# Kernel optimization log

Measured on AMD Instinct MI355X. Metric: run time of the kernel, lower is better.

The kernel has to match this reference:

```python
import jax, jax.numpy as jnp
import numpy as np

# NF4 codebook used by bitsandbytes (16 levels, normalized to [-1, 1])
NF4_CODE = jnp.array([
    -1.0, -0.6961928009986877, -0.5250730514526367, -0.39491748809814453,
    -0.28444138169288635, -0.18477343022823334, -0.09105003625154495, 0.0,
    0.07958029955625534, 0.16093020141124725, 0.24611230194568634,
    0.33791524171829224, 0.44070982933044434, 0.5626170039176941,
    0.7229568362236023, 1.0], dtype=jnp.float32)
BLOCKSIZE = 64  # bitsandbytes default 4-bit blocksize


def nf4_quant_dequant(w):
    """Simulate bnb NF4 quantize -> dequantize (per-block absmax scaling)."""
    shape = w.shape
    flat = w.reshape(-1, BLOCKSIZE)                     # [n_blocks, 64]
    absmax = jnp.max(jnp.abs(flat), axis=1, keepdims=True)
    normalized = flat / jnp.where(absmax == 0, 1.0, absmax)
    # nearest-codebook-value quantization via midpoint boundaries
    bounds = (NF4_CODE[:-1] + NF4_CODE[1:]) * 0.5       # [15]
    idx = jnp.searchsorted(bounds, normalized)          # [n_blocks, 64] in [0,15]
    return (NF4_CODE[idx] * absmax).reshape(shape)


def setup_inputs() -> dict:
    key = jax.random.key(0)
    k1, k2, k3, kx = jax.random.split(key, 4)
    D, H = 4096, 11008
    scale = 0.02  # typical transformer init scale
    w1 = jax.random.normal(k1, (H, D), jnp.float32) * scale
    w2 = jax.random.normal(k2, (H, D), jnp.float32) * scale
    w3 = jax.random.normal(k3, (D, H), jnp.float32) * scale
    x = jax.random.normal(kx, (2, 2048, D), jnp.float32)
    return {"x": x, "w1": w1, "w2": w2, "w3": w3}


def reference(x, w1, w2, w3):
    dq1 = nf4_quant_dequant(w1)   # [H, D]
    dq2 = nf4_quant_dequant(w2)   # [H, D]
    dq3 = nf4_quant_dequant(w3)   # [D, H]
    gate = jnp.einsum('bsd,hd->bsh', x, dq1)
    up = jnp.einsum('bsd,hd->bsh', x, dq2)
    h = jax.nn.silu(gate) * up
    return jnp.einsum('bsh,dh->bsd', h, dq3)
```

## Files before the change

### kernel.cpp

```cpp
#include <hip/hip_runtime.h>
#include <math.h>

typedef __attribute__((ext_vector_type(4))) float f32x4;
typedef __attribute__((ext_vector_type(8))) short bf16x8;

#define DI __device__ __forceinline__

DI unsigned short f32_to_bf16(float f) {
  unsigned int u = __float_as_uint(f);
  u += 0x7FFFu + ((u >> 16) & 1u);
  return (unsigned short)(u >> 16);
}

static constexpr float kCode[16] = {
    -1.0f, -0.6961928009986877f, -0.5250730514526367f, -0.39491748809814453f,
    -0.28444138169288635f, -0.18477343022823334f, -0.09105003625154495f, 0.0f,
    0.07958029955625534f, 0.16093020141124725f, 0.24611230194568634f,
    0.33791524171829224f, 0.44070982933044434f, 0.5626170039176941f,
    0.7229568362236023f, 1.0f};

__global__ void __launch_bounds__(256) k_dequant_nf4(
    const float* __restrict__ in, unsigned short* __restrict__ out, int n4) {
  int i = blockIdx.x * 256 + threadIdx.x;
  if (i >= n4) return;
  f32x4 v = reinterpret_cast<const f32x4*>(in)[i];
  float am = fmaxf(fmaxf(fabsf(v.x), fabsf(v.y)), fmaxf(fabsf(v.z), fabsf(v.w)));
  am = fmaxf(am, __shfl_xor(am, 1));
  am = fmaxf(am, __shfl_xor(am, 2));
  am = fmaxf(am, __shfl_xor(am, 4));
  am = fmaxf(am, __shfl_xor(am, 8));
  float scale = (am == 0.0f) ? 1.0f : am;
  unsigned short o[4];
#pragma unroll
  for (int j = 0; j < 4; ++j) {
    float nv = ((const float*)&v)[j] / scale;
    int idx = 0;
#pragma unroll
    for (int b = 0; b < 15; ++b)
      idx += (nv > 0.5f * (kCode[b] + kCode[b + 1])) ? 1 : 0;
    o[j] = f32_to_bf16(kCode[idx] * am);
  }
  reinterpret_cast<ushort4*>(out)[i] = make_ushort4(o[0], o[1], o[2], o[3]);
}

__global__ void __launch_bounds__(256) k_f32_to_bf16(
    const float* __restrict__ in, unsigned short* __restrict__ out, int n4) {
  int i = blockIdx.x * 256 + threadIdx.x;
  if (i >= n4) return;
  f32x4 v = reinterpret_cast<const f32x4*>(in)[i];
  reinterpret_cast<ushort4*>(out)[i] =
      make_ushort4(f32_to_bf16(v.x), f32_to_bf16(v.y), f32_to_bf16(v.z), f32_to_bf16(v.w));
}

DI void gload16(const void* g, void* l) {
  __builtin_amdgcn_global_load_lds(
      (const __attribute__((address_space(1))) void*)g,
      (__attribute__((address_space(3))) void*)l, 16, 0, 0);
}

DI void barrier_nodrain() {
  asm volatile("" ::: "memory");
  __builtin_amdgcn_s_barrier();
  asm volatile("" ::: "memory");
}

#define WAITV(N) asm volatile("s_waitcnt vmcnt(" #N ")" ::: "memory")

__global__ void __launch_bounds__(1024, 4) k_gemm_dual_swiglu(
    const unsigned short* __restrict__ X,
    const unsigned short* __restrict__ W1,
    const unsigned short* __restrict__ W2,
    unsigned short* __restrict__ H) {
  constexpr int K = 4096, N = 11008, NK = K / 32;
  __shared__ char ldsb[131072];

  const int tid = threadIdx.x;
  const int w = tid >> 6, l = tid & 63;

  const int bid = blockIdx.x;
  const int lt = (bid & 7) * 172 + (bid >> 3);
  const int mt = lt & 15, nt = lt >> 4;
  const int m0 = mt * 256, n0 = nt * 128;

  const int p = w & 7;
  const bool isGate = (w < 8);
  const int wr = p >> 1, wc = p & 1;

  const int lrow = l >> 2;
  const int kc8 = (((l & 3) ^ ((l >> 3) & 3)) << 3);
  const unsigned short* gsrc0;
  const unsigned short* gsrc1;
  int ldst0;
  if (w < 8) {
    gsrc0 = X + (size_t)(m0 + 32 * w + lrow) * K + kc8;
    gsrc1 = X + (size_t)(m0 + 32 * w + 16 + lrow) * K + kc8;
    ldst0 = 2 * w * 1024;
  } else if (w < 12) {
    gsrc0 = W1 + (size_t)(n0 + 32 * (w - 8) + lrow) * K + kc8;
    gsrc1 = W1 + (size_t)(n0 + 32 * (w - 8) + 16 + lrow) * K + kc8;
    ldst0 = 16384 + (w - 8) * 2048;
  } else {
    gsrc0 = W2 + (size_t)(n0 + 32 * (w - 12) + lrow) * K + kc8;
    gsrc1 = W2 + (size_t)(n0 + 32 * (w - 12) + 16 + lrow) * K + kc8;
    ldst0 = 24576 + (w - 12) * 2048;
  }

#define STG(t) { const int bo_ = (((t) & 3) << 15) + ldst0;          \
    gload16(gsrc0 + (size_t)(t) * 32, ldsb + bo_);                    \
    gload16(gsrc1 + (size_t)(t) * 32, ldsb + bo_ + 1024); }

  const int roff = (((l >> 4) ^ ((l >> 1) & 3)) << 4);
  const char* rdA = ldsb + (wr * 64 + (l & 15)) * 64 + roff;
  const char* rdB = ldsb + 16384 + (isGate ? 0 : 8192) +
                    (wc * 64 + (l & 15)) * 64 + roff;

  f32x4 acc[4][4] = {};

  STG(0); STG(1); STG(2);
  WAITV(4);
  barrier_nodrain();

  for (int t = 0; t < NK; ++t) {
    const int bo = (t & 3) << 15;
    if (t + 3 < NK) STG(t + 3);
    bf16x8 a[4], b[4];
#pragma unroll
    for (int m = 0; m < 4; ++m) a[m] = *(const bf16x8*)(rdA + bo + m * 1024);
#pragma unroll
    for (int n = 0; n < 4; ++n) b[n] = *(const bf16x8*)(rdB + bo + n * 1024);
    __builtin_amdgcn_s_setprio(1);
#pragma unroll
    for (int m = 0; m < 4; ++m)
#pragma unroll
      for (int n = 0; n < 4; ++n)
        acc[m][n] = __builtin_amdgcn_mfma_f32_16x16x32_bf16(a[m], b[n], acc[m][n], 0, 0, 0);
    __builtin_amdgcn_s_setprio(0);
    if (t + 3 < NK)      { WAITV(4); barrier_nodrain(); }
    else if (t + 2 < NK) { WAITV(2); barrier_nodrain(); }
    else if (t + 1 < NK) { WAITV(0); barrier_nodrain(); }
  }
#undef STG

  barrier_nodrain();
  char* xch = ldsb + p * 16384 + (isGate ? 0 : 8192);
#pragma unroll
  for (int m2 = 0; m2 < 2; ++m2)
#pragma unroll
    for (int n = 0; n < 4; ++n) {
      const int m = isGate ? (m2 + 2) : m2;
      *(f32x4*)(xch + ((m2 * 4 + n) * 64 + l) * 16) = acc[m][n];
    }
  barrier_nodrain();
  const char* oxch = ldsb + p * 16384 + (isGate ? 8192 : 0);
  const int er = (l >> 4) * 4, ec = l & 15;
#pragma unroll
  for (int m2 = 0; m2 < 2; ++m2)
#pragma unroll
    for (int n = 0; n < 4; ++n) {
      const int m = isGate ? m2 : (m2 + 2);
      f32x4 other = *(const f32x4*)(oxch + ((m2 * 4 + n) * 64 + l) * 16);
#pragma unroll
      for (int j = 0; j < 4; ++j) {
        const float g_ = isGate ? acc[m][n][j] : other[j];
        const float u_ = isGate ? other[j] : acc[m][n][j];
        const float s = g_ / (1.0f + expf(-g_));
        const int row = m0 + wr * 64 + m * 16 + er + j;
        const int col = n0 + wc * 64 + n * 16 + ec;
        H[(size_t)row * N + col] = f32_to_bf16(s * u_);
      }
    }
}

__global__ void __launch_bounds__(1024, 4) k_gemm_out(
    const unsigned short* __restrict__ Hm,
    const unsigned short* __restrict__ W3,
    float* __restrict__ Out) {
  constexpr int K = 11008, N = 4096, NK = K / 32;
  __shared__ char ldsb[131072];

  const int tid = threadIdx.x;
  const int w = tid >> 6, l = tid & 63;

  const int bid = blockIdx.x;
  const int lt = (bid & 7) * 32 + (bid >> 3);
  const int mt = lt & 15, nt = lt >> 4;
  const int m0 = mt * 256, n0 = nt * 256;

  const int wr = w >> 2, wc = w & 3;

  const int lrow = l >> 2;
  const int kc8 = (((l & 3) ^ ((l >> 3) & 3)) << 3);
  const unsigned short* gsrc0;
  const unsigned short* gsrc1;
  int ldst0;
  if (w < 8) {
    gsrc0 = Hm + (size_t)(m0 + 32 * w + lrow) * K + kc8;
    gsrc1 = Hm + (size_t)(m0 + 32 * w + 16 + lrow) * K + kc8;
    ldst0 = 2 * w * 1024;
  } else {
    gsrc0 = W3 + (size_t)(n0 + 32 * (w - 8) + lrow) * K + kc8;
    gsrc1 = W3 + (size_t)(n0 + 32 * (w - 8) + 16 + lrow) * K + kc8;
    ldst0 = 16384 + (w - 8) * 2048;
  }

#define STG(t) { const int bo_ = (((t) & 3) << 15) + ldst0;          \
    gload16(gsrc0 + (size_t)(t) * 32, ldsb + bo_);                    \
    gload16(gsrc1 + (size_t)(t) * 32, ldsb + bo_ + 1024); }

  const int roff = (((l >> 4) ^ ((l >> 1) & 3)) << 4);
  const char* rdA = ldsb + (wr * 64 + (l & 15)) * 64 + roff;
  const char* rdB = ldsb + 16384 + (wc * 64 + (l & 15)) * 64 + roff;

  f32x4 acc[4][4] = {};

  STG(0); STG(1); STG(2);
  WAITV(4);
  barrier_nodrain();

  for (int t = 0; t < NK; ++t) {
    const int bo = (t & 3) << 15;
    if (t + 3 < NK) STG(t + 3);
    bf16x8 a[4], b[4];
#pragma unroll
    for (int m = 0; m < 4; ++m) a[m] = *(const bf16x8*)(rdA + bo + m * 1024);
#pragma unroll
    for (int n = 0; n < 4; ++n) b[n] = *(const bf16x8*)(rdB + bo + n * 1024);
    __builtin_amdgcn_s_setprio(1);
#pragma unroll
    for (int m = 0; m < 4; ++m)
#pragma unroll
      for (int n = 0; n < 4; ++n)
        acc[m][n] = __builtin_amdgcn_mfma_f32_16x16x32_bf16(a[m], b[n], acc[m][n], 0, 0, 0);
    __builtin_amdgcn_s_setprio(0);
    if (t + 3 < NK)      { WAITV(4); barrier_nodrain(); }
    else if (t + 2 < NK) { WAITV(2); barrier_nodrain(); }
    else if (t + 1 < NK) { WAITV(0); barrier_nodrain(); }
  }
#undef STG

  const int er = (l >> 4) * 4, ec = l & 15;
#pragma unroll
  for (int m = 0; m < 4; ++m)
#pragma unroll
    for (int n = 0; n < 4; ++n) {
      const int row = m0 + wr * 64 + m * 16 + er;
      const int col = n0 + wc * 64 + n * 16 + ec;
      float* ptr = Out + (size_t)row * N + col;
#pragma unroll
      for (int j = 0; j < 4; ++j) ptr[(size_t)j * N] = acc[m][n][j];
    }
}

extern "C" void kernel_launch(void* const* d_in, const int* in_sizes, int n_in,
                              void* d_out, int out_size, void* d_ws, size_t ws_size,
                              hipStream_t stream) {
  const float* x  = (const float*)d_in[0];
  const float* w1 = (const float*)d_in[1];
  const float* w2 = (const float*)d_in[2];
  const float* w3 = (const float*)d_in[3];
  float* out = (float*)d_out;

  char* ws = (char*)d_ws;
  unsigned short* xb  = (unsigned short*)(ws);
  unsigned short* w1b = (unsigned short*)(ws + 33554432);
  unsigned short* w2b = (unsigned short*)(ws + 123731968);
  unsigned short* hb  = (unsigned short*)(ws + 213909504);
  unsigned short* w3b = w1b;

  const int NW = 11008 * 4096 / 4;
  k_f32_to_bf16<<<16384, 256, 0, stream>>>(x, xb, 4096 * 4096 / 4);
  k_dequant_nf4<<<NW / 256, 256, 0, stream>>>(w1, w1b, NW);
  k_dequant_nf4<<<NW / 256, 256, 0, stream>>>(w2, w2b, NW);

  k_gemm_dual_swiglu<<<1376, 1024, 0, stream>>>(xb, w1b, w2b, hb);

  k_dequant_nf4<<<NW / 256, 256, 0, stream>>>(w3, w3b, NW);

  k_gemm_out<<<256, 1024, 0, stream>>>(hb, w3b, out);
}
```

Measured before the change: 1.271 ms.

## Remap GEMM tiles per XCD, peel pipeline epilogue, merge w1/w2 dequant launches

Changes the block-to-tile mapping in both GEMMs so each XCD owns two consecutive M tiles and walks N tiles. The goal is L2 reuse of the activation rows within an XCD, instead of the earlier layout that spread M across XCDs. The main k-loop is peeled so the steady state carries no tail conditionals, and the two weight dequantization kernels are fused into one launch. The new tile order may reduce weight reuse across XCDs, since each XCD now streams all of W1/W2/W3.

New measurement: 1.247 ms. About the same (-1.9%).

```diff
diff --git a/kernel.cpp b/kernel.cpp
--- a/kernel.cpp
+++ b/kernel.cpp
@@ -19,10 +19,7 @@
     0.33791524171829224f, 0.44070982933044434f, 0.5626170039176941f,
     0.7229568362236023f, 1.0f};
 
-__global__ void __launch_bounds__(256) k_dequant_nf4(
-    const float* __restrict__ in, unsigned short* __restrict__ out, int n4) {
-  int i = blockIdx.x * 256 + threadIdx.x;
-  if (i >= n4) return;
+DI void dequant_body(const float* __restrict__ in, unsigned short* __restrict__ out, int i) {
   f32x4 v = reinterpret_cast<const f32x4*>(in)[i];
   float am = fmaxf(fmaxf(fabsf(v.x), fabsf(v.y)), fmaxf(fabsf(v.z), fabsf(v.w)));
   am = fmaxf(am, __shfl_xor(am, 1));
@@ -43,6 +40,24 @@
   reinterpret_cast<ushort4*>(out)[i] = make_ushort4(o[0], o[1], o[2], o[3]);
 }
 
+__global__ void __launch_bounds__(256) k_dequant_nf4(
+    const float* __restrict__ in, unsigned short* __restrict__ out, int n4) {
+  int i = blockIdx.x * 256 + threadIdx.x;
+  if (i >= n4) return;
+  dequant_body(in, out, i);
+}
+
+__global__ void __launch_bounds__(256) k_dequant_nf4_2(
+    const float* __restrict__ in1, const float* __restrict__ in2,
+    unsigned short* __restrict__ out1, unsigned short* __restrict__ out2, int n4) {
+  int i = blockIdx.x * 256 + threadIdx.x;
+  if (i < n4) {
+    dequant_body(in1, out1, i);
+  } else {
+    dequant_body(in2, out2, i - n4);
+  }
+}
+
 __global__ void __launch_bounds__(256) k_f32_to_bf16(
     const float* __restrict__ in, unsigned short* __restrict__ out, int n4) {
   int i = blockIdx.x * 256 + threadIdx.x;
@@ -78,8 +93,9 @@
   const int w = tid >> 6, l = tid & 63;
 
   const int bid = blockIdx.x;
-  const int lt = (bid & 7) * 172 + (bid >> 3);
-  const int mt = lt & 15, nt = lt >> 4;
+  const int xcd = bid & 7, i = bid >> 3;
+  const int nt = i >> 1;
+  const int mt = xcd * 2 + (i & 1);
   const int m0 = mt * 256, n0 = nt * 128;
 
   const int p = w & 7;
@@ -116,29 +132,33 @@
 
   f32x4 acc[4][4] = {};
 
+#define TILE_BODY(bo) {                                                        \
+  bf16x8 a[4], b[4];                                                           \
+  _Pragma("unroll") for (int m = 0; m < 4; ++m)                                \
+    a[m] = *(const bf16x8*)(rdA + (bo) + m * 1024);                            \
+  _Pragma("unroll") for (int n = 0; n < 4; ++n)                                \
+    b[n] = *(const bf16x8*)(rdB + (bo) + n * 1024);                            \
+  __builtin_amdgcn_s_setprio(1);                                               \
+  _Pragma("unroll") for (int m = 0; m < 4; ++m)                                \
+    _Pragma("unroll") for (int n = 0; n < 4; ++n)                              \
+      acc[m][n] = __builtin_amdgcn_mfma_f32_16x16x32_bf16(a[m], b[n], acc[m][n], 0, 0, 0); \
+  __builtin_amdgcn_s_setprio(0); }
+
   STG(0); STG(1); STG(2);
   WAITV(4);
   barrier_nodrain();
 
-  for (int t = 0; t < NK; ++t) {
+  int t = 0;
+  for (; t + 3 < NK; ++t) {
     const int bo = (t & 3) << 15;
-    if (t + 3 < NK) STG(t + 3);
-    bf16x8 a[4], b[4];
-#pragma unroll
-    for (int m = 0; m < 4; ++m) a[m] = *(const bf16x8*)(rdA + bo + m * 1024);
-#pragma unroll
-    for (int n = 0; n < 4; ++n) b[n] = *(const bf16x8*)(rdB + bo + n * 1024);
-    __builtin_amdgcn_s_setprio(1);
-#pragma unroll
-    for (int m = 0; m < 4; ++m)
-#pragma unroll
-      for (int n = 0; n < 4; ++n)
-        acc[m][n] = __builtin_amdgcn_mfma_f32_16x16x32_bf16(a[m], b[n], acc[m][n], 0, 0, 0);
-    __builtin_amdgcn_s_setprio(0);
-    if (t + 3 < NK)      { WAITV(4); barrier_nodrain(); }
-    else if (t + 2 < NK) { WAITV(2); barrier_nodrain(); }
-    else if (t + 1 < NK) { WAITV(0); barrier_nodrain(); }
-  }
+    STG(t + 3);
+    TILE_BODY(bo);
+    WAITV(4); barrier_nodrain();
+  }
+  TILE_BODY((t & 3) << 15); WAITV(2); barrier_nodrain(); ++t;
+  TILE_BODY((t & 3) << 15); WAITV(0); barrier_nodrain(); ++t;
+  TILE_BODY((t & 3) << 15);
+#undef TILE_BODY
 #undef STG
 
   barrier_nodrain();
@@ -157,14 +177,14 @@
   for (int m2 = 0; m2 < 2; ++m2)
 #pragma unroll
     for (int n = 0; n < 4; ++n) {
-      const int m = isGate ? m2 : (m2 + 2);
+      const int mk = isGate ? m2 : (m2 + 2);
       f32x4 other = *(const f32x4*)(oxch + ((m2 * 4 + n) * 64 + l) * 16);
 #pragma unroll
       for (int j = 0; j < 4; ++j) {
-        const float g_ = isGate ? acc[m][n][j] : other[j];
-        const float u_ = isGate ? other[j] : acc[m][n][j];
+        const float g_ = isGate ? acc[mk][n][j] : other[j];
+        const float u_ = isGate ? other[j] : acc[mk][n][j];
         const float s = g_ / (1.0f + expf(-g_));
-        const int row = m0 + wr * 64 + m * 16 + er + j;
+        const int row = m0 + wr * 64 + mk * 16 + er + j;
         const int col = n0 + wc * 64 + n * 16 + ec;
         H[(size_t)row * N + col] = f32_to_bf16(s * u_);
       }
@@ -182,8 +202,9 @@
   const int w = tid >> 6, l = tid & 63;
 
   const int bid = blockIdx.x;
-  const int lt = (bid & 7) * 32 + (bid >> 3);
-  const int mt = lt & 15, nt = lt >> 4;
+  const int xcd = bid & 7, i = bid >> 3;
+  const int nt = i >> 1;
+  const int mt = xcd * 2 + (i & 1);
   const int m0 = mt * 256, n0 = nt * 256;
 
   const int wr = w >> 2, wc = w & 3;
@@ -213,29 +234,33 @@
 
   f32x4 acc[4][4] = {};
 
+#define TILE_BODY(bo) {                                                        \
+  bf16x8 a[4], b[4];                                                           \
+  _Pragma("unroll") for (int m = 0; m < 4; ++m)                                \
+    a[m] = *(const bf16x8*)(rdA + (bo) + m * 1024);                            \
+  _Pragma("unroll") for (int n = 0; n < 4; ++n)                                \
+    b[n] = *(const bf16x8*)(rdB + (bo) + n * 1024);                            \
+  __builtin_amdgcn_s_setprio(1);                                               \
+  _Pragma("unroll") for (int m = 0; m < 4; ++m)                                \
+    _Pragma("unroll") for (int n = 0; n < 4; ++n)                              \
+      acc[m][n] = __builtin_amdgcn_mfma_f32_16x16x32_bf16(a[m], b[n], acc[m][n], 0, 0, 0); \
+  __builtin_amdgcn_s_setprio(0); }
+
   STG(0); STG(1); STG(2);
   WAITV(4);
   barrier_nodrain();
 
-  for (int t = 0; t < NK; ++t) {
+  int t = 0;
+  for (; t + 3 < NK; ++t) {
     const int bo = (t & 3) << 15;
-    if (t + 3 < NK) STG(t + 3);
-    bf16x8 a[4], b[4];
-#pragma unroll
-    for (int m = 0; m < 4; ++m) a[m] = *(const bf16x8*)(rdA + bo + m * 1024);
-#pragma unroll
-    for (int n = 0; n < 4; ++n) b[n] = *(const bf16x8*)(rdB + bo + n * 1024);
-    __builtin_amdgcn_s_setprio(1);
-#pragma unroll
-    for (int m = 0; m < 4; ++m)
-#pragma unroll
-      for (int n = 0; n < 4; ++n)
-        acc[m][n] = __builtin_amdgcn_mfma_f32_16x16x32_bf16(a[m], b[n], acc[m][n], 0, 0, 0);
-    __builtin_amdgcn_s_setprio(0);
-    if (t + 3 < NK)      { WAITV(4); barrier_nodrain(); }
-    else if (t + 2 < NK) { WAITV(2); barrier_nodrain(); }
-    else if (t + 1 < NK) { WAITV(0); barrier_nodrain(); }
-  }
+    STG(t + 3);
+    TILE_BODY(bo);
+    WAITV(4); barrier_nodrain();
+  }
+  TILE_BODY((t & 3) << 15); WAITV(2); barrier_nodrain(); ++t;
+  TILE_BODY((t & 3) << 15); WAITV(0); barrier_nodrain(); ++t;
+  TILE_BODY((t & 3) << 15);
+#undef TILE_BODY
 #undef STG
 
   const int er = (l >> 4) * 4, ec = l & 15;
@@ -269,8 +294,7 @@
 
   const int NW = 11008 * 4096 / 4;
   k_f32_to_bf16<<<16384, 256, 0, stream>>>(x, xb, 4096 * 4096 / 4);
-  k_dequant_nf4<<<NW / 256, 256, 0, stream>>>(w1, w1b, NW);
-  k_dequant_nf4<<<NW / 256, 256, 0, stream>>>(w2, w2b, NW);
+  k_dequant_nf4_2<<<2 * (NW / 256), 256, 0, stream>>>(w1, w2, w1b, w2b, NW);
 
   k_gemm_dual_swiglu<<<1376, 1024, 0, stream>>>(xb, w1b, w2b, hb);
 
```
